# Performance work log

Measured on AMD Instinct MI355X. Metric: run time of the kernel, lower is better.

The kernel has to match this reference:

```python
import jax, jax.numpy as jnp
import numpy as np
import math

B, T, D = 8, 1024, 1024
N, L = 256, 768
H = 16
TE = 2048  # time_embed_dim
EPS = 1e-5


def _ln(x, g, b):
    mu = jnp.mean(x, axis=-1, keepdims=True)
    var = jnp.mean(jnp.square(x - mu), axis=-1, keepdims=True)
    return (x - mu) * jax.lax.rsqrt(var + EPS) * g + b


def setup_inputs() -> dict:
    key = jax.random.key(0)
    ks = jax.random.split(key, 16)
    s = lambda fan_in: 1.0 / math.sqrt(fan_in)
    return {
        "x": jax.random.normal(ks[0], (B, T, D), jnp.float32),
        "xf": jax.random.normal(ks[1], (B, N, L), jnp.float32),
        "emb": jax.random.normal(ks[2], (B, TE), jnp.float32),
        "ln_g": jnp.ones((D,), jnp.float32),
        "ln_b": jnp.zeros((D,), jnp.float32),
        "cln_g": jnp.ones((L,), jnp.float32),
        "cln_b": jnp.zeros((L,), jnp.float32),
        "Wq": jax.random.normal(ks[3], (D, D), jnp.float32) * s(D),
        "bq": jnp.zeros((D,), jnp.float32),
        "Wk": jax.random.normal(ks[4], (L, D), jnp.float32) * s(L),
        "bk": jnp.zeros((D,), jnp.float32),
        "Wv": jax.random.normal(ks[5], (L, D), jnp.float32) * s(L),
        "bv": jnp.zeros((D,), jnp.float32),
        "sln_g": jnp.ones((D,), jnp.float32),
        "sln_b": jnp.zeros((D,), jnp.float32),
        "Wemb": jax.random.normal(ks[6], (TE, 2 * D), jnp.float32) * s(TE),
        "bemb": jnp.zeros((2 * D,), jnp.float32),
        "Wout": jax.random.normal(ks[7], (D, D), jnp.float32) * s(D) * 0.02,
        "bout": jnp.zeros((D,), jnp.float32),
    }


def reference(x, xf, emb, ln_g, ln_b, cln_g, cln_b, Wq, bq, Wk, bk, Wv, bv,
              sln_g, sln_b, Wemb, bemb, Wout, bout):
    # x: (B,T,D), xf: (B,N,L), emb: (B,TE)
    hd = D // H
    q = (_ln(x, ln_g, ln_b) @ Wq + bq).reshape(B, T, H, hd)
    xf_n = _ln(xf, cln_g, cln_b)
    k = (xf_n @ Wk + bk).reshape(B, N, H, hd)
    v = (xf_n @ Wv + bv).reshape(B, N, H, hd)
    # scores: (B,T,N,H); note: scaled by sqrt(D//H)
    att = jnp.einsum('bthd,bnhd->btnh', q, k) / math.sqrt(hd)
    w = jax.nn.softmax(att, axis=2)  # softmax over conditioning tokens N
    y = jnp.einsum('btnh,bnhd->bthd', w, v).reshape(B, T, D)
    # StylizationBlock (dropout = 0)
    emb_out = jax.nn.silu(emb) @ Wemb + bemb  # (B, 2D)
    scale, shift = jnp.split(emb_out[:, None, :], 2, axis=2)
    h = _ln(y, sln_g, sln_b) * (1.0 + scale) + shift
    h = jax.nn.silu(h) @ Wout + bout
    return x + h
```

## Files before the change

### kernel.cpp

```cpp
#include <hip/hip_runtime.h>
#include <hip/hip_bf16.h>

typedef __hip_bfloat16 bf16;
typedef unsigned short ushort;
typedef unsigned char uchar;
typedef long i64;
typedef __attribute__((ext_vector_type(8))) short bf16x8;
typedef __attribute__((ext_vector_type(4))) float f32x4;

#define B_ 8
#define T_ 1024
#define D_ 1024
#define N_ 256
#define L_ 768
#define H_ 16
#define HD_ 64
#define TE_ 2048

__device__ __forceinline__ void gld16(const void* g, void* l) {
    __builtin_amdgcn_global_load_lds((const __attribute__((address_space(1))) void*)g,
                                     (__attribute__((address_space(3))) void*)l,
                                     16, 0, 0);
}

__device__ __forceinline__ float bitf(unsigned u) { return __uint_as_float(u); }

__device__ __forceinline__ int pk4_fp8(float a, float b, float c, float d) {
    int p = __builtin_amdgcn_cvt_pk_fp8_f32(a, b, 0, false);
    p = __builtin_amdgcn_cvt_pk_fp8_f32(c, d, p, true);
    return p;
}
__device__ __forceinline__ uchar pk1_fp8(float a) {
    int p = __builtin_amdgcn_cvt_pk_fp8_f32(a, a, 0, false);
    return (uchar)(p & 0xff);
}

__global__ __launch_bounds__(256) void prep_kernel(
        const float* __restrict__ x, const float* __restrict__ xf,
        const float* __restrict__ g1, const float* __restrict__ b1,
        const float* __restrict__ g2, const float* __restrict__ b2,
        const float* __restrict__ Wq, const float* __restrict__ Wk,
        const float* __restrict__ Wv, const float* __restrict__ Wo,
        const float* __restrict__ emb, const float* __restrict__ Wemb,
        uchar* __restrict__ xn8, uchar* __restrict__ xfn8,
        uchar* __restrict__ wq8, uchar* __restrict__ wk8,
        uchar* __restrict__ wv8, uchar* __restrict__ wo8,
        float* __restrict__ part) {
    __shared__ __align__(16) char smem[16384];
    int bid = blockIdx.x;
    int tid = threadIdx.x;
    if (bid < 10240) {
        const float *rp, *g, *bb; uchar* op; int cols;
        if (bid < B_ * T_) {
            rp = x + (size_t)bid * D_; g = g1; bb = b1; op = xn8 + (size_t)bid * D_; cols = D_;
        } else {
            int r = bid - B_ * T_;
            rp = xf + (size_t)r * L_; g = g2; bb = b2; op = xfn8 + (size_t)r * L_; cols = L_;
        }
        float* ps  = (float*)smem;
        float* ps2 = ps + 4;
        float* st  = ps + 8;
        bool act = tid * 4 < cols;
        float4 v = act ? *(const float4*)&rp[tid * 4] : make_float4(0.f, 0.f, 0.f, 0.f);
        float s = v.x + v.y + v.z + v.w;
        float s2 = v.x * v.x + v.y * v.y + v.z * v.z + v.w * v.w;
        for (int off = 32; off; off >>= 1) {
            s  += __shfl_down(s,  off, 64);
            s2 += __shfl_down(s2, off, 64);
        }
        int wid = tid >> 6, lid = tid & 63;
        if (lid == 0) { ps[wid] = s; ps2[wid] = s2; }
        __syncthreads();
        if (tid == 0) {
            float t = ps[0] + ps[1] + ps[2] + ps[3];
            float t2 = ps2[0] + ps2[1] + ps2[2] + ps2[3];
            float m = t / cols;
            float var = t2 / cols - m * m;
            st[0] = m; st[1] = rsqrtf(var + 1e-5f);
        }
        __syncthreads();
        if (!act) return;
        float mu = st[0], rstd = st[1];
        float4 gv = *(const float4*)&g[tid * 4];
        float4 bv = *(const float4*)&bb[tid * 4];
        float o0 = (v.x - mu) * rstd * gv.x + bv.x;
        float o1 = (v.y - mu) * rstd * gv.y + bv.y;
        float o2 = (v.z - mu) * rstd * gv.z + bv.z;
        float o3 = (v.w - mu) * rstd * gv.w + bv.w;
        *(int*)&op[tid * 4] = pk4_fp8(o0, o1, o2, o3);
    } else if (bid < 11136) {
        uchar (*t)[65] = (uchar(*)[65])smem;
        int id = bid - 10240;
        int xb = id & 15, y = id >> 4;
        const float* W; uchar* Wt; int K, ky;
        if (y < 16)      { W = Wq; Wt = wq8; K = 1024; ky = y; }
        else if (y < 28) { W = Wk; Wt = wk8; K = 768;  ky = y - 16; }
        else if (y < 40) { W = Wv; Wt = wv8; K = 768;  ky = y - 28; }
        else             { W = Wo; Wt = wo8; K = 1024; ky = y - 40; }
        int k0 = ky * 64, n0 = xb * 64;
#pragma unroll
        for (int i = 0; i < 16; i++) {
            int e = tid + i * 256;
            int r = e >> 6, c = e & 63;
            t[r][c] = pk1_fp8(W[(size_t)(k0 + r) * D_ + n0 + c]);
        }
        __syncthreads();
#pragma unroll
        for (int i = 0; i < 4; i++) {
            int e = tid + i * 256;
            int r = e >> 4, cg = (e & 15) * 4;
            unsigned u = (unsigned)t[cg][r] | ((unsigned)t[cg + 1][r] << 8)
                       | ((unsigned)t[cg + 2][r] << 16) | ((unsigned)t[cg + 3][r] << 24);
            *(unsigned*)&Wt[(size_t)(n0 + r) * K + k0 + cg] = u;
        }
    } else {
        float* se  = (float*)smem;
        float* red = (float*)(smem + 8192);
        int id = bid - 11136;
        int j0 = (id & 31) * 64;
        int ks = id >> 5;
        int tx = tid & 15, ty = tid >> 4;
        int w = tid >> 6, lane = tid & 63;
#pragma unroll
        for (int b = 0; b < 8; b++) {
            float xv = emb[b * TE_ + ks * 256 + tid];
            se[b * 256 + tid] = xv / (1.f + __expf(-xv));
        }
        __syncthreads();
        float acc[8][4] = {};
#pragma unroll 4
        for (int i = 0; i < 16; i++) {
            int e = ty + 16 * i;
            float4 wv = *(const float4*)&Wemb[(size_t)(ks * 256 + e) * 2048 + j0 + tx * 4];
#pragma unroll
            for (int b = 0; b < 8; b++) {
                float s = se[b * 256 + e];
                acc[b][0] += s * wv.x; acc[b][1] += s * wv.y;
                acc[b][2] += s * wv.z; acc[b][3] += s * wv.w;
            }
        }
#pragma unroll
        for (int b = 0; b < 8; b++)
#pragma unroll
            for (int m = 0; m < 4; m++) {
                float v = acc[b][m];
                v += __shfl_down(v, 32, 64);
                v += __shfl_down(v, 16, 64);
                if (lane < 16) red[(w * 8 + b) * 64 + lane * 4 + m] = v;
            }
        __syncthreads();
        for (int o = tid; o < 512; o += 256) {
            int b = o >> 6, jl = o & 63;
            float s = red[(0 * 8 + b) * 64 + jl] + red[(1 * 8 + b) * 64 + jl]
                    + red[(2 * 8 + b) * 64 + jl] + red[(3 * 8 + b) * 64 + jl];
            part[((size_t)ks * 8 + b) * 2048 + j0 + jl] = s;
        }
    }
}

template <int MODE>
__device__ __forceinline__ void gemm_body(const uchar* __restrict__ Ap,
                                          const uchar* __restrict__ Bp,
                                          const float* __restrict__ bias,
                                          const float* __restrict__ res,
                                          void* __restrict__ Cout,
                                          int m0, int n0, int Ncols, int K,
                                          uchar* Ash, uchar* Bsh) {
    int tid = threadIdx.x;
    int w = tid >> 6, lane = tid & 63;
    int quad = lane >> 4, l15 = lane & 15;
    int wm = (w >> 1) * 64, wn = (w & 1) * 32;
    int lr8 = lane >> 3;
    int sc  = lane & 7;
    int gc  = sc ^ lr8;
    f32x4 acc[4][2] = {};
    for (int kt = 0; kt < K; kt += 128) {
#pragma unroll
        for (int j = 0; j < 4; j++) {
            int rbase = w * 32 + j * 8;
            gld16(&Ap[(size_t)(m0 + rbase + lr8) * K + kt + gc * 16], &Ash[rbase * 128]);
        }
#pragma unroll
        for (int j = 0; j < 2; j++) {
            int rbase = w * 16 + j * 8;
            gld16(&Bp[(size_t)(n0 + rbase + lr8) * K + kt + gc * 16], &Bsh[rbase * 128]);
        }
        __syncthreads();
#pragma unroll
        for (int kh = 0; kh < 4; kh++) {
            int c4 = kh * 2 + (quad >> 1);
            int sub = (quad & 1) * 8;
            int pos = (c4 ^ (l15 & 7)) * 16 + sub;
            i64 af[4], bfr[2];
#pragma unroll
            for (int mt = 0; mt < 4; mt++)
                af[mt] = *(const i64*)&Ash[(wm + mt * 16 + l15) * 128 + pos];
#pragma unroll
            for (int nt = 0; nt < 2; nt++)
                bfr[nt] = *(const i64*)&Bsh[(wn + nt * 16 + l15) * 128 + pos];
#pragma unroll
            for (int mt = 0; mt < 4; mt++)
#pragma unroll
                for (int nt = 0; nt < 2; nt++)
                    acc[mt][nt] = __builtin_amdgcn_mfma_f32_16x16x32_fp8_fp8(af[mt], bfr[nt], acc[mt][nt], 0, 0, 0);
        }
        __syncthreads();
    }
#pragma unroll
    for (int mt = 0; mt < 4; mt++) {
#pragma unroll
        for (int nt = 0; nt < 2; nt++) {
#pragma unroll
            for (int reg = 0; reg < 4; reg++) {
                int row = m0 + wm + mt * 16 + quad * 4 + reg;
                int col = n0 + wn + nt * 16 + l15;
                float v = acc[mt][nt][reg] + bias[col];
                if (MODE == 1) {
                    v += res[(size_t)row * Ncols + col];
                    ((float*)Cout)[(size_t)row * Ncols + col] = v;
                } else if (MODE == 0) {
                    ((bf16*)Cout)[(size_t)row * Ncols + col] = __float2bfloat16(v);
                } else {
                    int b = row >> 8, n = row & 255;
                    int h = col >> 6, d = col & 63;
                    size_t addr = ((size_t)(b * 16 + h) * 64 + d) * 256
                                + (((n >> 3) ^ (d & 7)) * 8) + (n & 7);
                    ((bf16*)Cout)[addr] = __float2bfloat16(v);
                }
            }
        }
    }
}

__global__ __launch_bounds__(256) void qkv_gemm(const uchar* __restrict__ xn8,
                                                const uchar* __restrict__ xfn8,
                                                const uchar* __restrict__ wq8,
                                                const uchar* __restrict__ wk8,
                                                const uchar* __restrict__ wv8,
                                                const float* __restrict__ bq,
                                                const float* __restrict__ bk,
                                                const float* __restrict__ bv,
                                                bf16* __restrict__ q,
                                                bf16* __restrict__ kbuf,
                                                bf16* __restrict__ vT,
                                                const float* __restrict__ part,
                                                const float* __restrict__ bemb,
                                                float* __restrict__ embo) {
    __shared__ __align__(16) uchar Ash[128 * 128];
    __shared__ __align__(16) uchar Bsh[64 * 128];
    int bid = blockIdx.x;
    if (bid < 1024) {
        gemm_body<0>(xn8, wq8, bq, nullptr, q,
                     (bid & 63) * 128, (bid >> 6) * 64, D_, D_, Ash, Bsh);
    } else if (bid < 1280) {
        int id = bid - 1024;
        gemm_body<0>(xfn8, wk8, bk, nullptr, kbuf,
                     (id & 15) * 128, (id >> 4) * 64, D_, L_, Ash, Bsh);
    } else if (bid < 1536) {
        int id = bid - 1280;
        gemm_body<2>(xfn8, wv8, bv, nullptr, vT,
                     (id & 15) * 128, (id >> 4) * 64, D_, L_, Ash, Bsh);
    } else {
        int o = (bid - 1536) * 256 + threadIdx.x;
        int b = o >> 11, j = o & 2047;
        float s = bemb[j];
#pragma unroll
        for (int ks = 0; ks < 8; ks++) s += part[((size_t)ks * 8 + b) * 2048 + j];
        embo[o] = s;
    }
}

__global__ __launch_bounds__(256) void out_gemm(const uchar* __restrict__ a8,
                                                const uchar* __restrict__ wo8,
                                                const float* __restrict__ bout,
                                                const float* __restrict__ x,
                                                float* __restrict__ out) {
    __shared__ __align__(16) uchar Ash[128 * 128];
    __shared__ __align__(16) uchar Bsh[64 * 128];
    int bid = blockIdx.x;
    gemm_body<1>(a8, wo8, bout, x, out,
                 (bid & 63) * 128, (bid >> 6) * 64, D_, D_, Ash, Bsh);
}

__global__ __launch_bounds__(256) void attn_mfma(const bf16* __restrict__ q,
                                                 const bf16* __restrict__ k,
                                                 const bf16* __restrict__ vT,
                                                 bf16* __restrict__ y) {
    __shared__ ushort KV[N_ * HD_];
    __shared__ ushort P[64 * N_];
    int tid = threadIdx.x;
    int w = tid >> 6, lane = tid & 63;
    int quad = lane >> 4, l15 = lane & 15;
    int t0 = blockIdx.x * 64;
    int bh = blockIdx.y;
    int b = bh >> 4, h = bh & 15;

    const ushort* kp = (const ushort*)k;
    const ushort* qp = (const ushort*)q;
    const ushort* vp = (const ushort*)vT;
    int lr8 = lane >> 3, sc = lane & 7, gc = sc ^ lr8;

#pragma unroll
    for (int j = 0; j < 8; j++) {
        int rbase = w * 64 + j * 8;
        gld16(&kp[(size_t)(b * N_ + rbase + lr8) * D_ + h * 64 + gc * 8], &KV[rbase * 64]);
    }
#pragma unroll
    for (int j = 0; j < 2; j++) {
        int rbase = w * 16 + j * 8;
        gld16(&qp[(size_t)(b * T_ + t0 + rbase + lr8) * D_ + h * 64 + gc * 8], &P[rbase * 64]);
    }
    __syncthreads();

    int qrow = w * 16 + l15;
    bf16x8 aq[2];
#pragma unroll
    for (int kk = 0; kk < 2; kk++)
        aq[kk] = *(bf16x8*)&P[qrow * 64 + (((kk * 4 + quad) ^ (qrow & 7)) * 8)];
    f32x4 sf[16];
#pragma unroll
    for (int nt = 0; nt < 16; nt++) {
        int n = nt * 16 + l15;
        bf16x8 b0 = *(bf16x8*)&KV[n * 64 + (((0 + quad) ^ (n & 7)) * 8)];
        bf16x8 b1 = *(bf16x8*)&KV[n * 64 + (((4 + quad) ^ (n & 7)) * 8)];
        f32x4 z = {};
        f32x4 t = __builtin_amdgcn_mfma_f32_16x16x32_bf16(aq[0], b0, z, 0, 0, 0);
        sf[nt] = __builtin_amdgcn_mfma_f32_16x16x32_bf16(aq[1], b1, t, 0, 0, 0);
    }
    __syncthreads();

    const ushort* vbase = vp + (size_t)(b * 16 + h) * 16384;
#pragma unroll
    for (int j = 0; j < 8; j++) {
        gld16(&vbase[(w * 8 + j) * 512 + lane * 8], &KV[(w * 8 + j) * 512]);
    }

    const float scale = 0.125f;
    float sm[4] = {0.f, 0.f, 0.f, 0.f};
#pragma unroll
    for (int nt = 0; nt < 16; nt++)
#pragma unroll
        for (int reg = 0; reg < 4; reg++) {
            float e = __expf(sf[nt][reg] * scale);
            sf[nt][reg] = e;
            sm[reg] += e;
        }
#pragma unroll
    for (int off = 1; off < 16; off <<= 1)
#pragma unroll
        for (int reg = 0; reg < 4; reg++)
            sm[reg] += __shfl_xor(sm[reg], off, 64);
    float inv[4];
#pragma unroll
    for (int reg = 0; reg < 4; reg++) inv[reg] = 1.f / sm[reg];

#pragma unroll
    for (int nt = 0; nt < 16; nt++)
#pragma unroll
        for (int reg = 0; reg < 4; reg++) {
            int r = w * 16 + quad * 4 + reg;
            int colc = nt * 2 + (l15 >> 3);
            int addr = r * 256 + ((colc ^ (r & 7)) * 8) + (l15 & 7);
            bf16 hv = __float2bfloat16(sf[nt][reg]);
            P[addr] = *(ushort*)&hv;
        }
    __syncthreads();

    f32x4 of[4] = {};
    int prow = w * 16 + l15;
#pragma unroll
    for (int kk = 0; kk < 8; kk++) {
        bf16x8 ap = *(bf16x8*)&P[prow * 256 + (((kk * 4 + quad) ^ (prow & 7)) * 8)];
#pragma unroll
        for (int dt = 0; dt < 4; dt++) {
            int d = dt * 16 + l15;
            bf16x8 bv = *(bf16x8*)&KV[d * 256 + (((kk * 4 + quad) ^ (d & 7)) * 8)];
            of[dt] = __builtin_amdgcn_mfma_f32_16x16x32_bf16(ap, bv, of[dt], 0, 0, 0);
        }
    }
#pragma unroll
    for (int dt = 0; dt < 4; dt++)
#pragma unroll
        for (int reg = 0; reg < 4; reg++) {
            int r = t0 + w * 16 + quad * 4 + reg;
            y[((size_t)(b * T_ + r) * D_) + h * 64 + dt * 16 + l15] =
                __float2bfloat16(of[dt][reg] * inv[reg]);
        }
}

__global__ __launch_bounds__(256) void styl_kernel(const bf16* __restrict__ y,
                                                   const float* __restrict__ g,
                                                   const float* __restrict__ bb,
                                                   const float* __restrict__ embo,
                                                   uchar* __restrict__ a8) {
    int row = blockIdx.x;
    int b = row >> 10;
    int tid = threadIdx.x;
    const ushort* rp = (const ushort*)(y + (size_t)row * D_);
    ushort4 uy = *(const ushort4*)&rp[tid * 4];
    float v0 = bitf((unsigned)uy.x << 16), v1 = bitf((unsigned)uy.y << 16);
    float v2 = bitf((unsigned)uy.z << 16), v3 = bitf((unsigned)uy.w << 16);
    float s = v0 + v1 + v2 + v3;
    float s2 = v0 * v0 + v1 * v1 + v2 * v2 + v3 * v3;
    for (int off = 32; off; off >>= 1) {
        s  += __shfl_down(s,  off, 64);
        s2 += __shfl_down(s2, off, 64);
    }
    __shared__ float ps[4], ps2[4];
    __shared__ float smu, srstd;
    int wid = tid >> 6, lid = tid & 63;
    if (lid == 0) { ps[wid] = s; ps2[wid] = s2; }
    __syncthreads();
    if (tid == 0) {
        float t = ps[0] + ps[1] + ps[2] + ps[3];
        float t2 = ps2[0] + ps2[1] + ps2[2] + ps2[3];
        float m = t / D_;
        float var = t2 / D_ - m * m;
        smu = m; srstd = rsqrtf(var + 1e-5f);
    }
    __syncthreads();
    float mu = smu, rstd = srstd;
    float4 gv = *(const float4*)&g[tid * 4];
    float4 bv = *(const float4*)&bb[tid * 4];
    float4 scv = *(const float4*)&embo[b * 2048 + tid * 4];
    float4 shv = *(const float4*)&embo[b * 2048 + 1024 + tid * 4];
    float n0 = (v0 - mu) * rstd * gv.x + bv.x;
    float n1 = (v1 - mu) * rstd * gv.y + bv.y;
    float n2 = (v2 - mu) * rstd * gv.z + bv.z;
    float n3 = (v3 - mu) * rstd * gv.w + bv.w;
    float h0 = n0 * (1.f + scv.x) + shv.x;
    float h1 = n1 * (1.f + scv.y) + shv.y;
    float h2 = n2 * (1.f + scv.z) + shv.z;
    float h3 = n3 * (1.f + scv.w) + shv.w;
    h0 = h0 / (1.f + __expf(-h0));
    h1 = h1 / (1.f + __expf(-h1));
    h2 = h2 / (1.f + __expf(-h2));
    h3 = h3 / (1.f + __expf(-h3));
    *(int*)&a8[(size_t)row * D_ + tid * 4] = pk4_fp8(h0, h1, h2, h3);
}

extern "C" void kernel_launch(void* const* d_in, const int* in_sizes, int n_in,
                              void* d_out, int out_size, void* d_ws, size_t ws_size,
                              hipStream_t stream) {
    const float* x    = (const float*)d_in[0];
    const float* xf   = (const float*)d_in[1];
    const float* emb  = (const float*)d_in[2];
    const float* ln_g = (const float*)d_in[3];
    const float* ln_b = (const float*)d_in[4];
    const float* cln_g= (const float*)d_in[5];
    const float* cln_b= (const float*)d_in[6];
    const float* Wq   = (const float*)d_in[7];
    const float* bq   = (const float*)d_in[8];
    const float* Wk   = (const float*)d_in[9];
    const float* bk   = (const float*)d_in[10];
    const float* Wv   = (const float*)d_in[11];
    const float* bv   = (const float*)d_in[12];
    const float* sln_g= (const float*)d_in[13];
    const float* sln_b= (const float*)d_in[14];
    const float* Wemb = (const float*)d_in[15];
    const float* bemb = (const float*)d_in[16];
    const float* Wout = (const float*)d_in[17];
    const float* bout = (const float*)d_in[18];
    float* out = (float*)d_out;

    char* wsp = (char*)d_ws;
    const size_t MB = 1024 * 1024;
    uchar* xn8  = (uchar*)(wsp);
    uchar* xfn8 = (uchar*)(wsp + 8 * MB);
    uchar* wq8  = (uchar*)(wsp + 10 * MB);
    uchar* wk8  = (uchar*)(wsp + 11 * MB);
    uchar* wv8  = (uchar*)(wsp + 12 * MB);
    uchar* wo8  = (uchar*)(wsp + 13 * MB);
    bf16*  q    = (bf16*)(wsp + 14 * MB);
    bf16*  kbuf = (bf16*)(wsp + 30 * MB);
    bf16*  vT   = (bf16*)(wsp + 34 * MB);
    bf16*  ybuf = (bf16*)(wsp + 38 * MB);
    uchar* a8   = (uchar*)(wsp + 54 * MB);
    float* embo = (float*)(wsp + 62 * MB);
    float* part = (float*)(wsp + 63 * MB);

    prep_kernel<<<11392, 256, 0, stream>>>(x, xf, ln_g, ln_b, cln_g, cln_b,
                                           Wq, Wk, Wv, Wout, emb, Wemb,
                                           xn8, xfn8, wq8, wk8, wv8, wo8, part);

    qkv_gemm<<<1600, 256, 0, stream>>>(xn8, xfn8, wq8, wk8, wv8, bq, bk, bv,
                                       q, kbuf, vT, part, bemb, embo);

    attn_mfma<<<dim3(16, 128), 256, 0, stream>>>(q, kbuf, vT, ybuf);

    styl_kernel<<<B_ * T_, 256, 0, stream>>>(ybuf, sln_g, sln_b, embo, a8);

    out_gemm<<<1024, 256, 0, stream>>>(a8, wo8, bout, x, out);
}
```

Measured before the change: 236.8 us.

## Store Q/K/V and attention output as fp8 and use fp8 MFMA in attention

```diff
diff --git a/kernel.cpp b/kernel.cpp
--- a/kernel.cpp
+++ b/kernel.cpp
@@ -5,7 +5,6 @@
 typedef unsigned short ushort;
 typedef unsigned char uchar;
 typedef long i64;
-typedef __attribute__((ext_vector_type(8))) short bf16x8;
 typedef __attribute__((ext_vector_type(4))) float f32x4;
 
 #define B_ 8
@@ -33,6 +32,12 @@
 __device__ __forceinline__ uchar pk1_fp8(float a) {
     int p = __builtin_amdgcn_cvt_pk_fp8_f32(a, a, 0, false);
     return (uchar)(p & 0xff);
+}
+__device__ __forceinline__ float dec8(uchar b) {
+    int e = (b >> 3) & 15, m = b & 7;
+    float mag = e ? (float)(8 + m) * bitf((unsigned)(117 + e) << 23)
+                  : (float)m * bitf(118u << 23);
+    return (b & 0x80) ? -mag : mag;
 }
 
 __global__ __launch_bounds__(256) void prep_kernel(
@@ -219,13 +224,13 @@
                     v += res[(size_t)row * Ncols + col];
                     ((float*)Cout)[(size_t)row * Ncols + col] = v;
                 } else if (MODE == 0) {
-                    ((bf16*)Cout)[(size_t)row * Ncols + col] = __float2bfloat16(v);
+                    ((uchar*)Cout)[(size_t)row * Ncols + col] = pk1_fp8(v);
                 } else {
                     int b = row >> 8, n = row & 255;
                     int h = col >> 6, d = col & 63;
-                    size_t addr = ((size_t)(b * 16 + h) * 64 + d) * 256
-                                + (((n >> 3) ^ (d & 7)) * 8) + (n & 7);
-                    ((bf16*)Cout)[addr] = __float2bfloat16(v);
+                    size_t addr = ((size_t)(b * 16 + h)) * 16384 + (size_t)d * 256
+                                + (((n >> 4) ^ (d & 15)) * 16) + (n & 15);
+                    ((uchar*)Cout)[addr] = pk1_fp8(v);
                 }
             }
         }
@@ -240,9 +245,9 @@
                                                 const float* __restrict__ bq,
                                                 const float* __restrict__ bk,
                                                 const float* __restrict__ bv,
-                                                bf16* __restrict__ q,
-                                                bf16* __restrict__ kbuf,
-                                                bf16* __restrict__ vT,
+                                                uchar* __restrict__ q8,
+                                                uchar* __restrict__ k8,
+                                                uchar* __restrict__ vT8,
                                                 const float* __restrict__ part,
                                                 const float* __restrict__ bemb,
                                                 float* __restrict__ embo) {
@@ -250,15 +255,15 @@
     __shared__ __align__(16) uchar Bsh[64 * 128];
     int bid = blockIdx.x;
     if (bid < 1024) {
-        gemm_body<0>(xn8, wq8, bq, nullptr, q,
+        gemm_body<0>(xn8, wq8, bq, nullptr, q8,
                      (bid & 63) * 128, (bid >> 6) * 64, D_, D_, Ash, Bsh);
     } else if (bid < 1280) {
         int id = bid - 1024;
-        gemm_body<0>(xfn8, wk8, bk, nullptr, kbuf,
+        gemm_body<0>(xfn8, wk8, bk, nullptr, k8,
                      (id & 15) * 128, (id >> 4) * 64, D_, L_, Ash, Bsh);
     } else if (bid < 1536) {
         int id = bid - 1280;
-        gemm_body<2>(xfn8, wv8, bv, nullptr, vT,
+        gemm_body<2>(xfn8, wv8, bv, nullptr, vT8,
                      (id & 15) * 128, (id >> 4) * 64, D_, L_, Ash, Bsh);
     } else {
         int o = (bid - 1536) * 256 + threadIdx.x;
@@ -282,57 +287,63 @@
                  (bid & 63) * 128, (bid >> 6) * 64, D_, D_, Ash, Bsh);
 }
 
-__global__ __launch_bounds__(256) void attn_mfma(const bf16* __restrict__ q,
-                                                 const bf16* __restrict__ k,
-                                                 const bf16* __restrict__ vT,
-                                                 bf16* __restrict__ y) {
-    __shared__ ushort KV[N_ * HD_];
-    __shared__ ushort P[64 * N_];
+__global__ __launch_bounds__(256) void attn_mfma(const uchar* __restrict__ q8,
+                                                 const uchar* __restrict__ k8,
+                                                 const uchar* __restrict__ vT8,
+                                                 uchar* __restrict__ y8) {
+    __shared__ __align__(16) uchar KV[16384];
+    __shared__ __align__(16) uchar P[16384];
     int tid = threadIdx.x;
     int w = tid >> 6, lane = tid & 63;
     int quad = lane >> 4, l15 = lane & 15;
     int t0 = blockIdx.x * 64;
     int bh = blockIdx.y;
     int b = bh >> 4, h = bh & 15;
-
-    const ushort* kp = (const ushort*)k;
-    const ushort* qp = (const ushort*)q;
-    const ushort* vp = (const ushort*)vT;
-    int lr8 = lane >> 3, sc = lane & 7, gc = sc ^ lr8;
-
-#pragma unroll
-    for (int j = 0; j < 8; j++) {
-        int rbase = w * 64 + j * 8;
-        gld16(&kp[(size_t)(b * N_ + rbase + lr8) * D_ + h * 64 + gc * 8], &KV[rbase * 64]);
+    int lln = lane >> 3, sp = lane & 7;
+
+#pragma unroll
+    for (int j = 0; j < 4; j++) {
+        int dn = w * 32 + j * 8 + lln;
+        int c8 = sp ^ (dn & 7);
+        int n = dn * 2 + (c8 >> 2);
+        gld16(&k8[(size_t)(b * N_ + n) * D_ + h * 64 + (c8 & 3) * 16],
+              &KV[(w * 32 + j * 8) * 128]);
     }
 #pragma unroll
     for (int j = 0; j < 2; j++) {
-        int rbase = w * 16 + j * 8;
-        gld16(&qp[(size_t)(b * T_ + t0 + rbase + lr8) * D_ + h * 64 + gc * 8], &P[rbase * 64]);
+        int r = w * 16 + j * 8 + lln;
+        int c = (sp ^ (r & 7)) & 3;
+        gld16(&q8[(size_t)(b * T_ + t0 + r) * D_ + h * 64 + c * 16],
+              &P[(w * 16 + j * 8) * 128]);
     }
     __syncthreads();
 
     int qrow = w * 16 + l15;
-    bf16x8 aq[2];
-#pragma unroll
-    for (int kk = 0; kk < 2; kk++)
-        aq[kk] = *(bf16x8*)&P[qrow * 64 + (((kk * 4 + quad) ^ (qrow & 7)) * 8)];
+    i64 aq[2];
+#pragma unroll
+    for (int kk2 = 0; kk2 < 2; kk2++) {
+        int chunk = kk2 * 2 + (quad >> 1);
+        aq[kk2] = *(const i64*)&P[qrow * 128 + ((chunk ^ (qrow & 7)) * 16) + (quad & 1) * 8];
+    }
     f32x4 sf[16];
 #pragma unroll
     for (int nt = 0; nt < 16; nt++) {
         int n = nt * 16 + l15;
-        bf16x8 b0 = *(bf16x8*)&KV[n * 64 + (((0 + quad) ^ (n & 7)) * 8)];
-        bf16x8 b1 = *(bf16x8*)&KV[n * 64 + (((4 + quad) ^ (n & 7)) * 8)];
+        int dn = n >> 1, hn = n & 1;
+        int c80 = (hn * 4 + 0 + (quad >> 1)) ^ (dn & 7);
+        int c81 = (hn * 4 + 2 + (quad >> 1)) ^ (dn & 7);
+        i64 b0 = *(const i64*)&KV[dn * 128 + c80 * 16 + (quad & 1) * 8];
+        i64 b1 = *(const i64*)&KV[dn * 128 + c81 * 16 + (quad & 1) * 8];
         f32x4 z = {};
-        f32x4 t = __builtin_amdgcn_mfma_f32_16x16x32_bf16(aq[0], b0, z, 0, 0, 0);
-        sf[nt] = __builtin_amdgcn_mfma_f32_16x16x32_bf16(aq[1], b1, t, 0, 0, 0);
+        f32x4 t = __builtin_amdgcn_mfma_f32_16x16x32_fp8_fp8(aq[0], b0, z, 0, 0, 0);
+        sf[nt] = __builtin_amdgcn_mfma_f32_16x16x32_fp8_fp8(aq[1], b1, t, 0, 0, 0);
     }
     __syncthreads();
 
-    const ushort* vbase = vp + (size_t)(b * 16 + h) * 16384;
-#pragma unroll
-    for (int j = 0; j < 8; j++) {
-        gld16(&vbase[(w * 8 + j) * 512 + lane * 8], &KV[(w * 8 + j) * 512]);
+    const uchar* vbase = vT8 + (size_t)(b * 16 + h) * 16384;
+#pragma unroll
+    for (int j = 0; j < 4; j++) {
+        gld16(&vbase[(w * 4 + j) * 1024 + lane * 16], &KV[(w * 4 + j) * 1024]);
     }
 
     const float scale = 0.125f;
@@ -359,10 +370,8 @@
 #pragma unroll
         for (int reg = 0; reg < 4; reg++) {
             int r = w * 16 + quad * 4 + reg;
-            int colc = nt * 2 + (l15 >> 3);
-            int addr = r * 256 + ((colc ^ (r & 7)) * 8) + (l15 & 7);
-            bf16 hv = __float2bfloat16(sf[nt][reg]);
-            P[addr] = *(ushort*)&hv;
+            int n = nt * 16 + l15;
+            P[r * 256 + (((n >> 4) ^ (r & 15)) * 16) + (n & 15)] = pk1_fp8(sf[nt][reg]);
         }
     __syncthreads();
 
@@ -370,12 +379,13 @@
     int prow = w * 16 + l15;
 #pragma unroll
     for (int kk = 0; kk < 8; kk++) {
-        bf16x8 ap = *(bf16x8*)&P[prow * 256 + (((kk * 4 + quad) ^ (prow & 7)) * 8)];
+        int ck = kk * 2 + (quad >> 1);
+        i64 ap = *(const i64*)&P[prow * 256 + ((ck ^ (prow & 15)) * 16) + (quad & 1) * 8];
 #pragma unroll
         for (int dt = 0; dt < 4; dt++) {
             int d = dt * 16 + l15;
-            bf16x8 bv = *(bf16x8*)&KV[d * 256 + (((kk * 4 + quad) ^ (d & 7)) * 8)];
-            of[dt] = __builtin_amdgcn_mfma_f32_16x16x32_bf16(ap, bv, of[dt], 0, 0, 0);
+            i64 bv = *(const i64*)&KV[d * 256 + ((ck ^ (d & 15)) * 16) + (quad & 1) * 8];
+            of[dt] = __builtin_amdgcn_mfma_f32_16x16x32_fp8_fp8(ap, bv, of[dt], 0, 0, 0);
         }
     }
 #pragma unroll
@@ -383,12 +393,12 @@
 #pragma unroll
         for (int reg = 0; reg < 4; reg++) {
             int r = t0 + w * 16 + quad * 4 + reg;
-            y[((size_t)(b * T_ + r) * D_) + h * 64 + dt * 16 + l15] =
-                __float2bfloat16(of[dt][reg] * inv[reg]);
-        }
-}
-
-__global__ __launch_bounds__(256) void styl_kernel(const bf16* __restrict__ y,
+            y8[(size_t)(b * T_ + r) * D_ + h * 64 + dt * 16 + l15] =
+                pk1_fp8(of[dt][reg] * inv[reg]);
+        }
+}
+
+__global__ __launch_bounds__(256) void styl_kernel(const uchar* __restrict__ y8,
                                                    const float* __restrict__ g,
                                                    const float* __restrict__ bb,
                                                    const float* __restrict__ embo,
@@ -396,10 +406,9 @@
     int row = blockIdx.x;
     int b = row >> 10;
     int tid = threadIdx.x;
-    const ushort* rp = (const ushort*)(y + (size_t)row * D_);
-    ushort4 uy = *(const ushort4*)&rp[tid * 4];
-    float v0 = bitf((unsigned)uy.x << 16), v1 = bitf((unsigned)uy.y << 16);
-    float v2 = bitf((unsigned)uy.z << 16), v3 = bitf((unsigned)uy.w << 16);
+    const uchar* rp = y8 + (size_t)row * D_;
+    uchar4 uy = *(const uchar4*)&rp[tid * 4];
+    float v0 = dec8(uy.x), v1 = dec8(uy.y), v2 = dec8(uy.z), v3 = dec8(uy.w);
     float s = v0 + v1 + v2 + v3;
     float s2 = v0 * v0 + v1 * v1 + v2 * v2 + v3 * v3;
     for (int off = 32; off; off >>= 1) {
@@ -471,24 +480,24 @@
     uchar* wk8  = (uchar*)(wsp + 11 * MB);
     uchar* wv8  = (uchar*)(wsp + 12 * MB);
     uchar* wo8  = (uchar*)(wsp + 13 * MB);
-    bf16*  q    = (bf16*)(wsp + 14 * MB);
-    bf16*  kbuf = (bf16*)(wsp + 30 * MB);
-    bf16*  vT   = (bf16*)(wsp + 34 * MB);
-    bf16*  ybuf = (bf16*)(wsp + 38 * MB);
-    uchar* a8   = (uchar*)(wsp + 54 * MB);
-    float* embo = (float*)(wsp + 62 * MB);
-    float* part = (float*)(wsp + 63 * MB);
+    uchar* q8   = (uchar*)(wsp + 14 * MB);
+    uchar* k8   = (uchar*)(wsp + 22 * MB);
+    uchar* vT8  = (uchar*)(wsp + 24 * MB);
+    uchar* y8   = (uchar*)(wsp + 26 * MB);
+    uchar* a8   = (uchar*)(wsp + 34 * MB);
+    float* embo = (float*)(wsp + 42 * MB);
+    float* part = (float*)(wsp + 43 * MB);
 
     prep_kernel<<<11392, 256, 0, stream>>>(x, xf, ln_g, ln_b, cln_g, cln_b,
                                            Wq, Wk, Wv, Wout, emb, Wemb,
                                            xn8, xfn8, wq8, wk8, wv8, wo8, part);
 
     qkv_gemm<<<1600, 256, 0, stream>>>(xn8, xfn8, wq8, wk8, wv8, bq, bk, bv,
-                                       q, kbuf, vT, part, bemb, embo);
-
-    attn_mfma<<<dim3(16, 128), 256, 0, stream>>>(q, kbuf, vT, ybuf);
-
-    styl_kernel<<<B_ * T_, 256, 0, stream>>>(ybuf, sln_g, sln_b, embo, a8);
+                                       q8, k8, vT8, part, bemb, embo);
+
+    attn_mfma<<<dim3(16, 128), 256, 0, stream>>>(q8, k8, vT8, y8);
+
+    styl_kernel<<<B_ * T_, 256, 0, stream>>>(y8, sln_g, sln_b, embo, a8);
 
     out_gemm<<<1024, 256, 0, stream>>>(a8, wo8, bout, x, out);
 }
```

New measurement: 231.2 us. -2.3%, faster.
